# Optimization experiments

Hardware: AMD Instinct MI355X
Metric: run time of the kernel (lower is better)

Reference implementation:

```python
import jax, jax.numpy as jnp
import numpy as np

B, T, H_IMG, HID, ACT = 128, 100, 72, 512, 2


def _conv(x, w, b, stride, pad):
    y = jax.lax.conv_general_dilated(
        x, w, (stride, stride), [(pad, pad), (pad, pad)],
        dimension_numbers=('NCHW', 'OIHW', 'NCHW'))
    return y + b[None, :, None, None]


def _encode(images, cw1, cb1, cw2, cb2, cw3, cb3, fw1, fb1, fw2, fb2, fw3, fb3):
    relu = jax.nn.relu
    x = relu(_conv(images, cw1, cb1, 3, 2))   # [B,64,24,24]
    x = relu(_conv(x, cw2, cb2, 3, 2))        # [B,64,9,9]
    x = relu(_conv(x, cw3, cb3, 3, 2))        # [B,64,4,4]
    x = x.reshape(x.shape[0], -1)             # [B,1024]
    x = relu(x @ fw1.T + fb1)
    x = relu(x @ fw2.T + fb2)
    return x @ fw3.T + fb3                    # [B,512]


def _gru(actions, h0, w_ih, w_hh, b_ih, b_hh):
    # precompute input projections for all steps: [T,B,3H]
    gi = jnp.einsum('btd,gd->tbg', actions, w_ih) + b_ih

    def step(h, gi_t):
        gh = h @ w_hh.T + b_hh
        i_r, i_i, i_n = jnp.split(gi_t, 3, axis=-1)
        h_r, h_i, h_n = jnp.split(gh, 3, axis=-1)
        r = jax.nn.sigmoid(i_r + h_r)
        z = jax.nn.sigmoid(i_i + h_i)
        n = jnp.tanh(i_n + r * h_n)
        hy = n + z * (h - n)
        return hy, hy

    hT, outs = jax.lax.scan(step, h0, gi)
    return jnp.transpose(outs, (1, 0, 2)), hT  # batch_first output


def setup_inputs() -> dict:
    key = jax.random.key(0)
    ks = jax.random.split(key, 16)
    s = 0.05
    return {
        'images': jax.random.normal(ks[0], (B, 3, H_IMG, H_IMG), jnp.float32),
        'actions': jax.random.normal(ks[1], (B, T, ACT), jnp.float32),
        'cw1': jax.random.normal(ks[2], (64, 3, 5, 5), jnp.float32) * s,
        'cb1': jax.random.normal(ks[3], (64,), jnp.float32) * s,
        'cw2': jax.random.normal(ks[4], (64, 64, 3, 3), jnp.float32) * s,
        'cb2': jax.random.normal(ks[5], (64,), jnp.float32) * s,
        'cw3': jax.random.normal(ks[6], (64, 64, 3, 3), jnp.float32) * s,
        'cb3': jax.random.normal(ks[7], (64,), jnp.float32) * s,
        'fw1': jax.random.normal(ks[8], (1024, 1024), jnp.float32) * 0.02,
        'fb1': jax.random.normal(ks[9], (1024,), jnp.float32) * 0.02,
        'fw2': jax.random.normal(ks[10], (512, 1024), jnp.float32) * 0.02,
        'fb2': jax.random.normal(ks[11], (512,), jnp.float32) * 0.02,
        'fw3': jax.random.normal(ks[12], (512, 512), jnp.float32) * 0.02,
        'fb3': jax.random.normal(ks[13], (512,), jnp.float32) * 0.02,
        'w_ih': jax.random.normal(ks[14], (3 * HID, ACT), jnp.float32) * 0.05,
        'w_hh': jax.random.normal(ks[15], (3 * HID, HID), jnp.float32) * 0.04,
        'b_ih': jnp.zeros((3 * HID,), jnp.float32),
        'b_hh': jnp.zeros((3 * HID,), jnp.float32),
    }


def reference(images, actions, cw1, cb1, cw2, cb2, cw3, cb3,
              fw1, fb1, fw2, fb2, fw3, fb3, w_ih, w_hh, b_ih, b_hh):
    # Encode the start image to a 512-d representation (BigBasicConv),
    # then integrate the action sequence with the hand-rolled GRU,
    # initial hidden state = start representation.
    h0 = _encode(images, cw1, cb1, cw2, cb2, cw3, cb3,
                 fw1, fb1, fw2, fb2, fw3, fb3)
    output, hT = _gru(actions, h0, w_ih, w_hh, b_ih, b_hh)
    return output, hT
```

## Files before the change

kernel.cpp:

```cpp
#include <hip/hip_runtime.h>
#include <cstdint>

#define BB   128
#define TT   100
#define HID  512

typedef __attribute__((ext_vector_type(4))) float f32x4;
typedef __attribute__((ext_vector_type(2))) float f32x2;
typedef __attribute__((ext_vector_type(8))) short short8;
typedef __attribute__((ext_vector_type(4))) short short4_t;

__device__ __forceinline__ short f2bf(float x) {
  unsigned u = __float_as_uint(x);
  unsigned r = (u + 0x7fffu + ((u >> 16) & 1u)) >> 16;
  return (short)r;
}
__device__ __forceinline__ float bf2f(short s) {
  return __uint_as_float(((unsigned)(unsigned short)s) << 16);
}

__global__ __launch_bounds__(256) void wsplit_k(const float* __restrict__ w,
                                                unsigned short* __restrict__ hi,
                                                unsigned short* __restrict__ lo,
                                                int nq) {
  int i = blockIdx.x * 256 + threadIdx.x;
  const int stride = gridDim.x * 256;
  for (; i < nq; i += stride) {
    f32x4 v = *(const f32x4*)(w + 4 * (long)i);
    short4_t h, l;
    #pragma unroll
    for (int c = 0; c < 4; c++) {
      short hh = f2bf(v[c]); h[c] = hh; l[c] = f2bf(v[c] - bf2f(hh));
    }
    *(short4_t*)(hi + 4 * (long)i) = h;
    *(short4_t*)(lo + 4 * (long)i) = l;
  }
}


__global__ __launch_bounds__(192) void conv1_k(const float* __restrict__ in,
                                               const float* __restrict__ w,
                                               const float* __restrict__ bias,
                                               float* __restrict__ out) {
  const int b = blockIdx.x / 24, oy = blockIdx.x % 24;
  __shared__ __attribute__((aligned(16))) float in_s[3][5][76];
  __shared__ __attribute__((aligned(16))) float ws[64][76];
  const int tid = threadIdx.x;
  for (int i = tid; i < 3 * 5 * 76; i += 192) {
    int ic = i / 380, rem = i % 380, r = rem / 76, p = rem % 76;
    int iy = oy * 3 + r - 2, ix = p - 2;
    in_s[ic][r][p] = (iy >= 0 && iy < 72 && ix >= 0 && ix < 72)
                       ? in[((long)(b * 3 + ic) * 72 + iy) * 72 + ix] : 0.f;
  }
  for (int i = tid; i < 64 * 75; i += 192) ws[i / 75][i % 75] = w[i];
  __syncthreads();

  const int ox2 = tid % 12;
  const int og = tid / 12;
  float strip[15][8];
  #pragma unroll
  for (int ic = 0; ic < 3; ic++)
    #pragma unroll
    for (int ky = 0; ky < 5; ky++) {
      const float* bp = &in_s[ic][ky][6 * ox2];
      #pragma unroll
      for (int h = 0; h < 4; h++) {
        f32x2 u = *(const f32x2*)(bp + 2 * h);
        strip[ic * 5 + ky][2 * h] = u[0];
        strip[ic * 5 + ky][2 * h + 1] = u[1];
      }
    }

  #pragma unroll
  for (int j = 0; j < 4; j++) {
    const int oc = og + 16 * j;
    float s0 = bias[oc], s1 = bias[oc];
    const float* wrow = ws[oc];
    #pragma unroll
    for (int k4 = 0; k4 < 18; k4++) {
      f32x4 wq = *(const f32x4*)(wrow + 4 * k4);
      #pragma unroll
      for (int q = 0; q < 4; q++) {
        const int k = 4 * k4 + q, i5 = k / 5, kx = k % 5;
        s0 += strip[i5][kx] * wq[q];
        s1 += strip[i5][kx + 3] * wq[q];
      }
    }
    s0 += strip[14][2] * wrow[72]; s1 += strip[14][5] * wrow[72];
    s0 += strip[14][3] * wrow[73]; s1 += strip[14][6] * wrow[73];
    s0 += strip[14][4] * wrow[74]; s1 += strip[14][7] * wrow[74];
    long o = ((long)(b * 64 + oc) * 24 + oy) * 24 + 2 * ox2;
    out[o] = fmaxf(s0, 0.f);
    out[o + 1] = fmaxf(s1, 0.f);
  }
}

template <int IC, int IH, int IW, int OC, int OH, int OW>
__global__ void convs3(const float* __restrict__ in, const float* __restrict__ w,
                       const float* __restrict__ bias, float* __restrict__ out) {
  const int b = blockIdx.x / OH, oy = blockIdx.x % OH;
  constexpr int PW = 3 * OW;
  constexpr int NT = (OC / 2) * OW;
  __shared__ __attribute__((aligned(16))) float in_s[8][3][PW];
  __shared__ __attribute__((aligned(16))) float w_s[OC][100];
  const int tid = threadIdx.x;
  const int oc = tid / OW, ox = tid % OW;
  float s0 = bias[oc], s1 = bias[oc + OC / 2];
  for (int cc = 0; cc < IC; cc += 8) {
    __syncthreads();
    for (int i = tid; i < 8 * 3 * PW; i += NT) {
      int ic = i / (3 * PW), r = (i / PW) % 3, p = i % PW;
      int iy = oy * 3 - 2 + r, ix = p - 2;
      in_s[ic][r][p] = (iy >= 0 && iy < IH && ix >= 0 && ix < IW)
                         ? in[((long)(b * IC + cc + ic) * IH + iy) * IW + ix] : 0.f;
    }
    for (int i = tid; i < OC * 8 * 9; i += NT) {
      int o = i / 72, r = i % 72;
      w_s[o][(r / 9) * 12 + (r % 9)] = w[(long)(o * IC + cc + r / 9) * 9 + r % 9];
    }
    __syncthreads();
    #pragma unroll
    for (int ic = 0; ic < 8; ic++) {
      const float* wr0 = &w_s[oc][ic * 12];
      const float* wr1 = &w_s[oc + OC / 2][ic * 12];
      f32x4 wa = *(const f32x4*)wr0, wb = *(const f32x4*)(wr0 + 4);
      f32x4 va = *(const f32x4*)wr1, vb = *(const f32x4*)(wr1 + 4);
      float wA[9] = {wa[0], wa[1], wa[2], wa[3], wb[0], wb[1], wb[2], wb[3], wr0[8]};
      float wB[9] = {va[0], va[1], va[2], va[3], vb[0], vb[1], vb[2], vb[3], wr1[8]};
      #pragma unroll
      for (int ky = 0; ky < 3; ky++)
        #pragma unroll
        for (int kx = 0; kx < 3; kx++) {
          float iv = in_s[ic][ky][ox * 3 + kx];
          s0 += iv * wA[ky * 3 + kx];
          s1 += iv * wB[ky * 3 + kx];
        }
    }
  }
  out[((long)(b * OC + oc) * OH + oy) * OW + ox] = fmaxf(s0, 0.f);
  out[((long)(b * OC + oc + OC / 2) * OH + oy) * OW + ox] = fmaxf(s1, 0.f);
}

template <int K, int N, bool RELU>
__global__ __launch_bounds__(128) void fc_mfma(const float* __restrict__ A,
                                               const unsigned short* __restrict__ wh,
                                               const unsigned short* __restrict__ wl,
                                               const float* __restrict__ bias,
                                               float* __restrict__ C) {
  const int nb = N / 32;
  const int rb = (blockIdx.x / nb) * 16, cb = (blockIdx.x % nb) * 32;
  __shared__ __attribute__((aligned(16))) short A_hi[16][K + 8];
  __shared__ __attribute__((aligned(16))) short A_lo[16][K + 8];
  const int tid = threadIdx.x;
  const int wv = tid >> 6, lane = tid & 63, n16 = lane & 15, quad = lane >> 4;

  for (int i = tid; i < 16 * (K / 4); i += 128) {
    int row = i / (K / 4), q = i % (K / 4);
    f32x4 v = *(const f32x4*)(A + (long)(rb + row) * K + 4 * q);
    short4_t sh, sl;
    #pragma unroll
    for (int c = 0; c < 4; c++) {
      short hh = f2bf(v[c]); sh[c] = hh; sl[c] = f2bf(v[c] - bf2f(hh));
    }
    *(short4_t*)&A_hi[row][4 * q] = sh;
    *(short4_t*)&A_lo[row][4 * q] = sl;
  }
  __syncthreads();

  const int col = cb + wv * 16 + n16;
  f32x4 a0 = {0.f, 0.f, 0.f, 0.f}, a1 = a0, a2 = a0;
  constexpr int NP = K / 512;
  #pragma unroll 1
  for (int p = 0; p < NP; p++) {
    short8 fh[16], fl[16];
    const unsigned short* wb0 = wh + (long)col * K + p * 512 + quad * 8;
    const unsigned short* wb1 = wl + (long)col * K + p * 512 + quad * 8;
    #pragma unroll
    for (int ks = 0; ks < 16; ks++) {
      fh[ks] = *(const short8*)(wb0 + ks * 32);
      fl[ks] = *(const short8*)(wb1 + ks * 32);
    }
    #pragma unroll
    for (int ks = 0; ks < 16; ks++) {
      short8 ah = *(const short8*)&A_hi[n16][p * 512 + ks * 32 + quad * 8];
      short8 al = *(const short8*)&A_lo[n16][p * 512 + ks * 32 + quad * 8];
      a0 = __builtin_amdgcn_mfma_f32_16x16x32_bf16(ah, fh[ks], a0, 0, 0, 0);
      a1 = __builtin_amdgcn_mfma_f32_16x16x32_bf16(al, fh[ks], a1, 0, 0, 0);
      a2 = __builtin_amdgcn_mfma_f32_16x16x32_bf16(ah, fl[ks], a2, 0, 0, 0);
    }
  }
  const float bv = bias[col];
  #pragma unroll
  for (int r = 0; r < 4; r++) {
    float v = a0[r] + a1[r] + a2[r] + bv;
    if (RELU) v = fmaxf(v, 0.f);
    C[(long)(rb + quad * 4 + r) * N + col] = v;
  }
}

__global__ __launch_bounds__(192, 1) void gru_k(
    const float* __restrict__ actions, const float* __restrict__ w_ih,
    const float* __restrict__ w_hh, const float* __restrict__ b_ih,
    const float* __restrict__ b_hh, const float* __restrict__ h0,
    float* __restrict__ out, float* __restrict__ hT, unsigned* __restrict__ bar) {
  const int bg = blockIdx.x >> 5;
  const int hg = blockIdx.x & 31;
  const int tid = threadIdx.x;
  const int wv = tid >> 6;
  const int lane = tid & 63;
  const int n16 = lane & 15;
  const int quad = lane >> 4;

  __shared__ short h_hi[16][520];
  __shared__ short h_lo[16][520];
  __shared__ float act_s[16][2 * TT];
  __shared__ float gh_s[3][16][17];
  __shared__ float bih_s[48], bhh_s[48], wih0_s[48], wih1_s[48];

  short8 whi[16], wlo[16];
  {
    const int grow = wv * HID + hg * 16 + n16;
    const float* wr = w_hh + (long)grow * HID + quad * 8;
    #pragma unroll
    for (int ks = 0; ks < 16; ks++) {
      f32x4 v0 = *(const f32x4*)(wr + ks * 32);
      f32x4 v1 = *(const f32x4*)(wr + ks * 32 + 4);
      short8 hi, lo;
      #pragma unroll
      for (int j = 0; j < 4; j++) {
        short h1 = f2bf(v0[j]); hi[j] = h1;     lo[j] = f2bf(v0[j] - bf2f(h1));
        short h2 = f2bf(v1[j]); hi[j + 4] = h2; lo[j + 4] = f2bf(v1[j] - bf2f(h2));
      }
      whi[ks] = hi; wlo[ks] = lo;
    }
  }
  for (int i = tid; i < 48; i += 192) {
    int row = (i >> 4) * HID + hg * 16 + (i & 15);
    bih_s[i] = b_ih[row];
    bhh_s[i] = b_hh[row];
    wih0_s[i] = w_ih[row * 2];
    wih1_s[i] = w_ih[row * 2 + 1];
  }
  for (int i = tid; i < 16 * 2 * TT; i += 192) {
    int m = i / (2 * TT), r = i % (2 * TT);
    act_s[m][r] = actions[(long)(bg * 16 + m) * (2 * TT) + r];
  }
  for (int i = tid; i < 2048; i += 192) {
    int m = i >> 7, k4 = (i & 127) << 2;
    f32x4 v = *(const f32x4*)(h0 + (long)(bg * 16 + m) * HID + k4);
    short4_t sh, sl;
    #pragma unroll
    for (int c2 = 0; c2 < 4; c2++) {
      short hh = f2bf(v[c2]); sh[c2] = hh; sl[c2] = f2bf(v[c2] - bf2f(hh));
    }
    *(short4_t*)&h_hi[m][k4] = sh;
    *(short4_t*)&h_lo[m][k4] = sl;
  }
  __syncthreads();

  unsigned* my_bar = bar + bg * 32;

  #pragma unroll 1
  for (int t = 0; t < TT; t++) {
    f32x4 a0 = {0.f, 0.f, 0.f, 0.f}, a1 = a0, a2 = a0;
    #pragma unroll
    for (int ks = 0; ks < 16; ks++) {
      short8 ah = *(const short8*)&h_hi[n16][ks * 32 + quad * 8];
      short8 al = *(const short8*)&h_lo[n16][ks * 32 + quad * 8];
      a0 = __builtin_amdgcn_mfma_f32_16x16x32_bf16(ah, whi[ks], a0, 0, 0, 0);
      a1 = __builtin_amdgcn_mfma_f32_16x16x32_bf16(al, whi[ks], a1, 0, 0, 0);
      a2 = __builtin_amdgcn_mfma_f32_16x16x32_bf16(ah, wlo[ks], a2, 0, 0, 0);
    }
    #pragma unroll
    for (int r = 0; r < 4; r++)
      gh_s[wv][quad * 4 + r][n16] = a0[r] + a1[r] + a2[r];
    __syncthreads();

    if (tid < 128) {
      const int m = tid >> 3;
      const int n0 = (tid & 7) << 1;
      const float x0 = act_s[m][2 * t], x1 = act_s[m][2 * t + 1];
      float hy[2];
      #pragma unroll
      for (int q = 0; q < 2; q++) {
        int n = n0 + q;
        float hr = gh_s[0][m][n] + bhh_s[n];
        float hz = gh_s[1][m][n] + bhh_s[16 + n];
        float hn = gh_s[2][m][n] + bhh_s[32 + n];
        float ir = x0 * wih0_s[n]      + x1 * wih1_s[n]      + bih_s[n];
        float iz = x0 * wih0_s[16 + n] + x1 * wih1_s[16 + n] + bih_s[16 + n];
        float in_ = x0 * wih0_s[32 + n] + x1 * wih1_s[32 + n] + bih_s[32 + n];
        float rg = 1.f / (1.f + __expf(-(ir + hr)));
        float zg = 1.f / (1.f + __expf(-(iz + hz)));
        float nx = in_ + rg * hn;
        float ng = 1.f - 2.f / (__expf(2.f * nx) + 1.f);
        float hprev = bf2f(h_hi[m][hg * 16 + n]) + bf2f(h_lo[m][hg * 16 + n]);
        hy[q] = ng + zg * (hprev - ng);
      }
      unsigned long long pack = (unsigned long long)__float_as_uint(hy[0]) |
                                ((unsigned long long)__float_as_uint(hy[1]) << 32);
      __hip_atomic_store(
          (unsigned long long*)&out[((long)(bg * 16 + m) * TT + t) * HID + hg * 16 + n0],
          pack, __ATOMIC_RELAXED, __HIP_MEMORY_SCOPE_AGENT);
      if (t == TT - 1)
        *(unsigned long long*)&hT[(long)(bg * 16 + m) * HID + hg * 16 + n0] = pack;
    }
    __syncthreads();

    if (t < TT - 1) {
      if (tid == 0) {
        const unsigned target = 32u * (unsigned)(t + 1);
        unsigned prev = __hip_atomic_fetch_add(my_bar, 1u, __ATOMIC_RELAXED,
                                               __HIP_MEMORY_SCOPE_AGENT);
        if (prev + 1u < target) {
          while (__hip_atomic_load(my_bar, __ATOMIC_RELAXED,
                                   __HIP_MEMORY_SCOPE_AGENT) < target)
            __builtin_amdgcn_s_sleep(1);
        }
      }
      __syncthreads();
      unsigned long long vbuf[22];
      #pragma unroll
      for (int u = 0; u < 21; u++) {
        int i = tid + u * 192;
        int m = i >> 8, j = (i & 255) << 1;
        vbuf[u] = __hip_atomic_load(
            (const unsigned long long*)(out + ((long)(bg * 16 + m) * TT + t) * HID + j),
            __ATOMIC_RELAXED, __HIP_MEMORY_SCOPE_AGENT);
      }
      if (tid < 64) {
        int i = 4032 + tid;
        int m = i >> 8, j = (i & 255) << 1;
        vbuf[21] = __hip_atomic_load(
            (const unsigned long long*)(out + ((long)(bg * 16 + m) * TT + t) * HID + j),
            __ATOMIC_RELAXED, __HIP_MEMORY_SCOPE_AGENT);
      }
      #pragma unroll
      for (int u = 0; u < 21; u++) {
        int i = tid + u * 192;
        int m = i >> 8, j = (i & 255) << 1;
        unsigned long long v = vbuf[u];
        float f0 = __uint_as_float((unsigned)v);
        float f1 = __uint_as_float((unsigned)(v >> 32));
        short s0 = f2bf(f0);
        h_hi[m][j] = s0; h_lo[m][j] = f2bf(f0 - bf2f(s0));
        short s1 = f2bf(f1);
        h_hi[m][j + 1] = s1; h_lo[m][j + 1] = f2bf(f1 - bf2f(s1));
      }
      if (tid < 64) {
        int i = 4032 + tid;
        int m = i >> 8, j = (i & 255) << 1;
        unsigned long long v = vbuf[21];
        float f0 = __uint_as_float((unsigned)v);
        float f1 = __uint_as_float((unsigned)(v >> 32));
        short s0 = f2bf(f0);
        h_hi[m][j] = s0; h_lo[m][j] = f2bf(f0 - bf2f(s0));
        short s1 = f2bf(f1);
        h_hi[m][j + 1] = s1; h_lo[m][j + 1] = f2bf(f1 - bf2f(s1));
      }
      __syncthreads();
    }
  }
}

extern "C" void kernel_launch(void* const* d_in, const int* in_sizes, int n_in,
                              void* d_out, int out_size, void* d_ws, size_t ws_size,
                              hipStream_t stream) {
  const float* images  = (const float*)d_in[0];
  const float* actions = (const float*)d_in[1];
  const float* cw1 = (const float*)d_in[2];
  const float* cb1 = (const float*)d_in[3];
  const float* cw2 = (const float*)d_in[4];
  const float* cb2 = (const float*)d_in[5];
  const float* cw3 = (const float*)d_in[6];
  const float* cb3 = (const float*)d_in[7];
  const float* fw1 = (const float*)d_in[8];
  const float* fb1 = (const float*)d_in[9];
  const float* fw2 = (const float*)d_in[10];
  const float* fb2 = (const float*)d_in[11];
  const float* fw3 = (const float*)d_in[12];
  const float* fb3 = (const float*)d_in[13];
  const float* w_ih = (const float*)d_in[14];
  const float* w_hh = (const float*)d_in[15];
  const float* b_ih = (const float*)d_in[16];
  const float* b_hh = (const float*)d_in[17];

  char* ws = (char*)d_ws;
  unsigned* bar = (unsigned*)ws;
  float* a1 = (float*)(ws + 1024);
  float* a2 = a1 + (long)128 * 64 * 576;
  float* a3 = a2 + (long)128 * 64 * 81;
  float* f1 = a3 + (long)128 * 1024;
  float* f2 = f1 + (long)128 * 1024;
  float* h0 = f2 + (long)128 * 512;
  unsigned short* wfh1 = (unsigned short*)(h0 + 65536);
  unsigned short* wfl1 = wfh1 + (long)1048576;
  unsigned short* wfh2 = wfl1 + (long)1048576;
  unsigned short* wfl2 = wfh2 + (long)524288;
  unsigned short* wfh3 = wfl2 + (long)524288;
  unsigned short* wfl3 = wfh3 + (long)262144;

  float* out = (float*)d_out;
  float* hT  = out + (long)BB * TT * HID;

  hipMemsetAsync(bar, 0, 1024, stream);
  wsplit_k<<<256, 256, 0, stream>>>(fw1, wfh1, wfl1, 262144);
  wsplit_k<<<128, 256, 0, stream>>>(fw2, wfh2, wfl2, 131072);
  wsplit_k<<<64, 256, 0, stream>>>(fw3, wfh3, wfl3, 65536);
  conv1_k<<<128 * 24, 192, 0, stream>>>(images, cw1, cb1, a1);
  convs3<64, 24, 24, 64, 9, 9><<<128 * 9, 288, 0, stream>>>(a1, cw2, cb2, a2);
  convs3<64, 9, 9, 64, 4, 4><<<128 * 4, 128, 0, stream>>>(a2, cw3, cb3, a3);
  fc_mfma<1024, 1024, true><<<256, 128, 0, stream>>>(a3, wfh1, wfl1, fb1, f1);
  fc_mfma<1024, 512, true><<<128, 128, 0, stream>>>(f1, wfh2, wfl2, fb2, f2);
  fc_mfma<512, 512, false><<<128, 128, 0, stream>>>(f2, wfh3, wfl3, fb3, h0);
  gru_k<<<256, 192, 0, stream>>>(actions, w_ih, w_hh, b_ih, b_hh, h0, out, hT, bar);
}
```

Before: 645.1 us.

## Exchange GRU hidden state as pre-split bf16 planes read directly into MFMA fragments

Each GRU block now publishes its new hidden slice as double-buffered bf16 hi/lo planes in global memory. The next step loads the MFMA A-fragments straight from those planes, which removes the per-step fp32 reload of the full hidden state, the bf16 split and the LDS staging pass. Work across the three waves is also rearranged: wave 0 multiplies h_hi by W_hi, wave 1 h_lo by W_hi and wave 2 h_hi by W_lo, each covering all three gates, and the partial sums are added in shared memory. Previous hidden values stay in registers, and an extra wsplit launch splits h0 into hi/lo. The cost is more weight registers per wave and uncached agent-scope global loads sitting on the critical path of every step.

```diff
diff --git a/kernel.cpp b/kernel.cpp
--- a/kernel.cpp
+++ b/kernel.cpp
@@ -202,36 +202,41 @@
     const float* __restrict__ actions, const float* __restrict__ w_ih,
     const float* __restrict__ w_hh, const float* __restrict__ b_ih,
     const float* __restrict__ b_hh, const float* __restrict__ h0,
-    float* __restrict__ out, float* __restrict__ hT, unsigned* __restrict__ bar) {
+    float* __restrict__ out, float* __restrict__ hT, unsigned* __restrict__ bar,
+    unsigned short* __restrict__ xh, unsigned short* __restrict__ xl) {
   const int bg = blockIdx.x >> 5;
   const int hg = blockIdx.x & 31;
   const int tid = threadIdx.x;
-  const int wv = tid >> 6;
+  const int ch = tid >> 6;
   const int lane = tid & 63;
   const int n16 = lane & 15;
   const int quad = lane >> 4;
-
-  __shared__ short h_hi[16][520];
-  __shared__ short h_lo[16][520];
+  const long PLANE = (long)BB * HID;
+
   __shared__ float act_s[16][2 * TT];
-  __shared__ float gh_s[3][16][17];
+  __shared__ float gh_s[3][16][52];
   __shared__ float bih_s[48], bhh_s[48], wih0_s[48], wih1_s[48];
 
-  short8 whi[16], wlo[16];
+  short8 wfrag[3][16];
   {
-    const int grow = wv * HID + hg * 16 + n16;
-    const float* wr = w_hh + (long)grow * HID + quad * 8;
-    #pragma unroll
-    for (int ks = 0; ks < 16; ks++) {
-      f32x4 v0 = *(const f32x4*)(wr + ks * 32);
-      f32x4 v1 = *(const f32x4*)(wr + ks * 32 + 4);
-      short8 hi, lo;
+    #pragma unroll
+    for (int g = 0; g < 3; g++) {
+      const int grow = g * HID + hg * 16 + n16;
+      const float* wr = w_hh + (long)grow * HID + quad * 8;
       #pragma unroll
-      for (int j = 0; j < 4; j++) {
-        short h1 = f2bf(v0[j]); hi[j] = h1;     lo[j] = f2bf(v0[j] - bf2f(h1));
-        short h2 = f2bf(v1[j]); hi[j + 4] = h2; lo[j + 4] = f2bf(v1[j] - bf2f(h2));
-      }
-      whi[ks] = hi; wlo[ks] = lo;
+      for (int ks = 0; ks < 16; ks++) {
+        f32x4 v0 = *(const f32x4*)(wr + ks * 32);
+        f32x4 v1 = *(const f32x4*)(wr + ks * 32 + 4);
+        short8 f;
+        #pragma unroll
+        for (int j = 0; j < 4; j++) {
+          float x0 = v0[j], x1 = v1[j];
+          short hh0 = f2bf(x0), hh1 = f2bf(x1);
+          f[j]     = (ch == 2) ? f2bf(x0 - bf2f(hh0)) : hh0;
+          f[j + 4] = (ch == 2) ? f2bf(x1 - bf2f(hh1)) : hh1;
+        }
+        wfrag[g][ks] = f;
+      }
     }
   }
   for (int i = tid; i < 48; i += 192) {
@@ -245,35 +250,45 @@
     int m = i / (2 * TT), r = i % (2 * TT);
     act_s[m][r] = actions[(long)(bg * 16 + m) * (2 * TT) + r];
   }
-  for (int i = tid; i < 2048; i += 192) {
-    int m = i >> 7, k4 = (i & 127) << 2;
-    f32x4 v = *(const f32x4*)(h0 + (long)(bg * 16 + m) * HID + k4);
-    short4_t sh, sl;
-    #pragma unroll
-    for (int c2 = 0; c2 < 4; c2++) {
-      short hh = f2bf(v[c2]); sh[c2] = hh; sl[c2] = f2bf(v[c2] - bf2f(hh));
-    }
-    *(short4_t*)&h_hi[m][k4] = sh;
-    *(short4_t*)&h_lo[m][k4] = sl;
+  float hp0 = 0.f, hp1 = 0.f;
+  if (tid < 128) {
+    const int m = tid >> 3, n0 = (tid & 7) << 1;
+    f32x2 u = *(const f32x2*)(h0 + (long)(bg * 16 + m) * HID + hg * 16 + n0);
+    hp0 = u[0]; hp1 = u[1];
   }
   __syncthreads();
 
   unsigned* my_bar = bar + bg * 32;
+  const unsigned short* xa = (ch == 1) ? xl : xh;
+  const long lane_off = ((long)(bg * 16 + n16) << 9) + quad * 8;
 
   #pragma unroll 1
   for (int t = 0; t < TT; t++) {
+    const unsigned long long* fp =
+        (const unsigned long long*)(xa + (t & 1) * PLANE + lane_off);
+    unsigned long long fb[16][2];
+    #pragma unroll
+    for (int ks = 0; ks < 16; ks++) {
+      fb[ks][0] = __hip_atomic_load(fp + ks * 8, __ATOMIC_RELAXED,
+                                    __HIP_MEMORY_SCOPE_AGENT);
+      fb[ks][1] = __hip_atomic_load(fp + ks * 8 + 1, __ATOMIC_RELAXED,
+                                    __HIP_MEMORY_SCOPE_AGENT);
+    }
     f32x4 a0 = {0.f, 0.f, 0.f, 0.f}, a1 = a0, a2 = a0;
     #pragma unroll
     for (int ks = 0; ks < 16; ks++) {
-      short8 ah = *(const short8*)&h_hi[n16][ks * 32 + quad * 8];
-      short8 al = *(const short8*)&h_lo[n16][ks * 32 + quad * 8];
-      a0 = __builtin_amdgcn_mfma_f32_16x16x32_bf16(ah, whi[ks], a0, 0, 0, 0);
-      a1 = __builtin_amdgcn_mfma_f32_16x16x32_bf16(al, whi[ks], a1, 0, 0, 0);
-      a2 = __builtin_amdgcn_mfma_f32_16x16x32_bf16(ah, wlo[ks], a2, 0, 0, 0);
-    }
-    #pragma unroll
-    for (int r = 0; r < 4; r++)
-      gh_s[wv][quad * 4 + r][n16] = a0[r] + a1[r] + a2[r];
+      union { unsigned long long q[2]; short8 s; } u;
+      u.q[0] = fb[ks][0]; u.q[1] = fb[ks][1];
+      a0 = __builtin_amdgcn_mfma_f32_16x16x32_bf16(u.s, wfrag[0][ks], a0, 0, 0, 0);
+      a1 = __builtin_amdgcn_mfma_f32_16x16x32_bf16(u.s, wfrag[1][ks], a1, 0, 0, 0);
+      a2 = __builtin_amdgcn_mfma_f32_16x16x32_bf16(u.s, wfrag[2][ks], a2, 0, 0, 0);
+    }
+    #pragma unroll
+    for (int r = 0; r < 4; r++) {
+      gh_s[ch][quad * 4 + r][n16]      = a0[r];
+      gh_s[ch][quad * 4 + r][16 + n16] = a1[r];
+      gh_s[ch][quad * 4 + r][32 + n16] = a2[r];
+    }
     __syncthreads();
 
     if (tid < 128) {
@@ -284,9 +299,9 @@
       #pragma unroll
       for (int q = 0; q < 2; q++) {
         int n = n0 + q;
-        float hr = gh_s[0][m][n] + bhh_s[n];
-        float hz = gh_s[1][m][n] + bhh_s[16 + n];
-        float hn = gh_s[2][m][n] + bhh_s[32 + n];
+        float hr = gh_s[0][m][n]      + gh_s[1][m][n]      + gh_s[2][m][n]      + bhh_s[n];
+        float hz = gh_s[0][m][16 + n] + gh_s[1][m][16 + n] + gh_s[2][m][16 + n] + bhh_s[16 + n];
+        float hn = gh_s[0][m][32 + n] + gh_s[1][m][32 + n] + gh_s[2][m][32 + n] + bhh_s[32 + n];
         float ir = x0 * wih0_s[n]      + x1 * wih1_s[n]      + bih_s[n];
         float iz = x0 * wih0_s[16 + n] + x1 * wih1_s[16 + n] + bih_s[16 + n];
         float in_ = x0 * wih0_s[32 + n] + x1 * wih1_s[32 + n] + bih_s[32 + n];
@@ -294,16 +309,29 @@
         float zg = 1.f / (1.f + __expf(-(iz + hz)));
         float nx = in_ + rg * hn;
         float ng = 1.f - 2.f / (__expf(2.f * nx) + 1.f);
-        float hprev = bf2f(h_hi[m][hg * 16 + n]) + bf2f(h_lo[m][hg * 16 + n]);
+        float hprev = q ? hp1 : hp0;
         hy[q] = ng + zg * (hprev - ng);
       }
+      hp0 = hy[0]; hp1 = hy[1];
       unsigned long long pack = (unsigned long long)__float_as_uint(hy[0]) |
                                 ((unsigned long long)__float_as_uint(hy[1]) << 32);
-      __hip_atomic_store(
-          (unsigned long long*)&out[((long)(bg * 16 + m) * TT + t) * HID + hg * 16 + n0],
-          pack, __ATOMIC_RELAXED, __HIP_MEMORY_SCOPE_AGENT);
-      if (t == TT - 1)
+      *(unsigned long long*)&out[((long)(bg * 16 + m) * TT + t) * HID + hg * 16 + n0] = pack;
+      if (t == TT - 1) {
         *(unsigned long long*)&hT[(long)(bg * 16 + m) * HID + hg * 16 + n0] = pack;
+      } else {
+        short s0h = f2bf(hy[0]), s1h = f2bf(hy[1]);
+        short s0l = f2bf(hy[0] - bf2f(s0h)), s1l = f2bf(hy[1] - bf2f(s1h));
+        unsigned hpk = (unsigned)(unsigned short)s0h |
+                       ((unsigned)(unsigned short)s1h << 16);
+        unsigned lpk = (unsigned)(unsigned short)s0l |
+                       ((unsigned)(unsigned short)s1l << 16);
+        const long xo = ((t + 1) & 1) * PLANE +
+                        ((long)(bg * 16 + m) << 9) + hg * 16 + n0;
+        __hip_atomic_store((unsigned*)(xh + xo), hpk, __ATOMIC_RELAXED,
+                           __HIP_MEMORY_SCOPE_AGENT);
+        __hip_atomic_store((unsigned*)(xl + xo), lpk, __ATOMIC_RELAXED,
+                           __HIP_MEMORY_SCOPE_AGENT);
+      }
     }
     __syncthreads();
 
@@ -317,46 +345,6 @@
                                    __HIP_MEMORY_SCOPE_AGENT) < target)
             __builtin_amdgcn_s_sleep(1);
         }
-      }
-      __syncthreads();
-      unsigned long long vbuf[22];
-      #pragma unroll
-      for (int u = 0; u < 21; u++) {
-        int i = tid + u * 192;
-        int m = i >> 8, j = (i & 255) << 1;
-        vbuf[u] = __hip_atomic_load(
-            (const unsigned long long*)(out + ((long)(bg * 16 + m) * TT + t) * HID + j),
-            __ATOMIC_RELAXED, __HIP_MEMORY_SCOPE_AGENT);
-      }
-      if (tid < 64) {
-        int i = 4032 + tid;
-        int m = i >> 8, j = (i & 255) << 1;
-        vbuf[21] = __hip_atomic_load(
-            (const unsigned long long*)(out + ((long)(bg * 16 + m) * TT + t) * HID + j),
-            __ATOMIC_RELAXED, __HIP_MEMORY_SCOPE_AGENT);
-      }
-      #pragma unroll
-      for (int u = 0; u < 21; u++) {
-        int i = tid + u * 192;
-        int m = i >> 8, j = (i & 255) << 1;
-        unsigned long long v = vbuf[u];
-        float f0 = __uint_as_float((unsigned)v);
-        float f1 = __uint_as_float((unsigned)(v >> 32));
-        short s0 = f2bf(f0);
-        h_hi[m][j] = s0; h_lo[m][j] = f2bf(f0 - bf2f(s0));
-        short s1 = f2bf(f1);
-        h_hi[m][j + 1] = s1; h_lo[m][j + 1] = f2bf(f1 - bf2f(s1));
-      }
-      if (tid < 64) {
-        int i = 4032 + tid;
-        int m = i >> 8, j = (i & 255) << 1;
-        unsigned long long v = vbuf[21];
-        float f0 = __uint_as_float((unsigned)v);
-        float f1 = __uint_as_float((unsigned)(v >> 32));
-        short s0 = f2bf(f0);
-        h_hi[m][j] = s0; h_lo[m][j] = f2bf(f0 - bf2f(s0));
-        short s1 = f2bf(f1);
-        h_hi[m][j + 1] = s1; h_lo[m][j + 1] = f2bf(f1 - bf2f(s1));
       }
       __syncthreads();
     }
@@ -399,6 +387,8 @@
   unsigned short* wfl2 = wfh2 + (long)524288;
   unsigned short* wfh3 = wfl2 + (long)524288;
   unsigned short* wfl3 = wfh3 + (long)262144;
+  unsigned short* xh = wfl3 + (long)262144;
+  unsigned short* xl = xh + (long)2 * 128 * 512;
 
   float* out = (float*)d_out;
   float* hT  = out + (long)BB * TT * HID;
@@ -413,5 +403,7 @@
   fc_mfma<1024, 1024, true><<<256, 128, 0, stream>>>(a3, wfh1, wfl1, fb1, f1);
   fc_mfma<1024, 512, true><<<128, 128, 0, stream>>>(f1, wfh2, wfl2, fb2, f2);
   fc_mfma<512, 512, false><<<128, 128, 0, stream>>>(f2, wfh3, wfl3, fb3, h0);
-  gru_k<<<256, 192, 0, stream>>>(actions, w_ih, w_hh, b_ih, b_hh, h0, out, hT, bar);
-}
+  wsplit_k<<<64, 256, 0, stream>>>(h0, xh, xl, 16384);
+  gru_k<<<256, 192, 0, stream>>>(actions, w_ih, w_hh, b_ih, b_hh, h0, out, hT,
+                                 bar, xh, xl);
+}
```

Result: slower. 783.2 us (+21.4%).

## Replace GRU atomic counter barrier with tagged double-buffered hidden-state exchange

Applied to the files above, without the earlier changes.

Drops the per-batch-group atomic counter barrier and the extra __syncthreads between GRU steps. Each block now publishes its new hidden-state slice to a double-buffered exchange buffer, pre-split into bf16 hi/lo pairs with a parity tag bit in the low mantissa bit. Consumers poll the tagged words directly until every tag matches, then unpack them into shared memory without redoing the split. The previous hidden value is also kept in registers instead of being rebuilt from shared memory. The cost is one low bit of the lo part per element and a second global write stream alongside the out writes.

```diff
diff --git a/kernel.cpp b/kernel.cpp
--- a/kernel.cpp
+++ b/kernel.cpp
@@ -9,6 +9,7 @@
 typedef __attribute__((ext_vector_type(2))) float f32x2;
 typedef __attribute__((ext_vector_type(8))) short short8;
 typedef __attribute__((ext_vector_type(4))) short short4_t;
+typedef unsigned long long ull;
 
 __device__ __forceinline__ short f2bf(float x) {
   unsigned u = __float_as_uint(x);
@@ -202,7 +203,8 @@
     const float* __restrict__ actions, const float* __restrict__ w_ih,
     const float* __restrict__ w_hh, const float* __restrict__ b_ih,
     const float* __restrict__ b_hh, const float* __restrict__ h0,
-    float* __restrict__ out, float* __restrict__ hT, unsigned* __restrict__ bar) {
+    float* __restrict__ out, float* __restrict__ hT,
+    unsigned* __restrict__ xb) {
   const int bg = blockIdx.x >> 5;
   const int hg = blockIdx.x & 31;
   const int tid = threadIdx.x;
@@ -256,9 +258,13 @@
     *(short4_t*)&h_hi[m][k4] = sh;
     *(short4_t*)&h_lo[m][k4] = sl;
   }
+  float hp0 = 0.f, hp1 = 0.f;
+  if (tid < 128) {
+    const int m = tid >> 3, n0 = (tid & 7) << 1;
+    f32x2 u = *(const f32x2*)(h0 + (long)(bg * 16 + m) * HID + hg * 16 + n0);
+    hp0 = u[0]; hp1 = u[1];
+  }
   __syncthreads();
-
-  unsigned* my_bar = bar + bg * 32;
 
   #pragma unroll 1
   for (int t = 0; t < TT; t++) {
@@ -275,6 +281,10 @@
     for (int r = 0; r < 4; r++)
       gh_s[wv][quad * 4 + r][n16] = a0[r] + a1[r] + a2[r];
     __syncthreads();
+
+    const int nt = t + 1;
+    const unsigned tagbit = (unsigned)((nt >> 1) & 1);
+    unsigned* xcur = xb + (nt & 1) * 65536;
 
     if (tid < 128) {
       const int m = tid >> 3;
@@ -294,69 +304,75 @@
         float zg = 1.f / (1.f + __expf(-(iz + hz)));
         float nx = in_ + rg * hn;
         float ng = 1.f - 2.f / (__expf(2.f * nx) + 1.f);
-        float hprev = bf2f(h_hi[m][hg * 16 + n]) + bf2f(h_lo[m][hg * 16 + n]);
+        float hprev = q ? hp1 : hp0;
         hy[q] = ng + zg * (hprev - ng);
       }
-      unsigned long long pack = (unsigned long long)__float_as_uint(hy[0]) |
-                                ((unsigned long long)__float_as_uint(hy[1]) << 32);
-      __hip_atomic_store(
-          (unsigned long long*)&out[((long)(bg * 16 + m) * TT + t) * HID + hg * 16 + n0],
-          pack, __ATOMIC_RELAXED, __HIP_MEMORY_SCOPE_AGENT);
-      if (t == TT - 1)
-        *(unsigned long long*)&hT[(long)(bg * 16 + m) * HID + hg * 16 + n0] = pack;
-    }
-    __syncthreads();
+      hp0 = hy[0]; hp1 = hy[1];
+      ull pack = (ull)__float_as_uint(hy[0]) |
+                 ((ull)__float_as_uint(hy[1]) << 32);
+      *(ull*)&out[((long)(bg * 16 + m) * TT + t) * HID + hg * 16 + n0] = pack;
+      if (t == TT - 1) {
+        *(ull*)&hT[(long)(bg * 16 + m) * HID + hg * 16 + n0] = pack;
+      } else {
+        short s0h = f2bf(hy[0]), s1h = f2bf(hy[1]);
+        short s0l = f2bf(hy[0] - bf2f(s0h)), s1l = f2bf(hy[1] - bf2f(s1h));
+        unsigned w0 = ((unsigned)(unsigned short)s0h << 16) |
+                      (((unsigned)(unsigned short)s0l) & 0xFFFEu) | tagbit;
+        unsigned w1 = ((unsigned)(unsigned short)s1h << 16) |
+                      (((unsigned)(unsigned short)s1l) & 0xFFFEu) | tagbit;
+        ull pk = (ull)w0 | ((ull)w1 << 32);
+        __hip_atomic_store(
+            (ull*)xcur + ((long)bg * 4096 + m * 256 + hg * 8 + (n0 >> 1)),
+            pk, __ATOMIC_RELAXED, __HIP_MEMORY_SCOPE_AGENT);
+      }
+    }
 
     if (t < TT - 1) {
-      if (tid == 0) {
-        const unsigned target = 32u * (unsigned)(t + 1);
-        unsigned prev = __hip_atomic_fetch_add(my_bar, 1u, __ATOMIC_RELAXED,
-                                               __HIP_MEMORY_SCOPE_AGENT);
-        if (prev + 1u < target) {
-          while (__hip_atomic_load(my_bar, __ATOMIC_RELAXED,
-                                   __HIP_MEMORY_SCOPE_AGENT) < target)
-            __builtin_amdgcn_s_sleep(1);
+      const ull* xq = (const ull*)xcur + (long)bg * 4096;
+      ull vb[22];
+      #pragma unroll
+      for (int u = 0; u < 21; u++)
+        vb[u] = __hip_atomic_load(xq + tid + u * 192, __ATOMIC_RELAXED,
+                                  __HIP_MEMORY_SCOPE_AGENT);
+      if (tid < 64)
+        vb[21] = __hip_atomic_load(xq + 4032 + tid, __ATOMIC_RELAXED,
+                                   __HIP_MEMORY_SCOPE_AGENT);
+      for (;;) {
+        unsigned bad = 0;
+        #pragma unroll
+        for (int u = 0; u < 21; u++) {
+          unsigned lo32 = (unsigned)vb[u], hi32 = (unsigned)(vb[u] >> 32);
+          if ((((lo32 ^ tagbit) | (hi32 ^ tagbit)) & 1u) != 0u) {
+            vb[u] = __hip_atomic_load(xq + tid + u * 192, __ATOMIC_RELAXED,
+                                      __HIP_MEMORY_SCOPE_AGENT);
+            bad = 1u;
+          }
         }
-      }
-      __syncthreads();
-      unsigned long long vbuf[22];
+        if (tid < 64) {
+          unsigned lo32 = (unsigned)vb[21], hi32 = (unsigned)(vb[21] >> 32);
+          if ((((lo32 ^ tagbit) | (hi32 ^ tagbit)) & 1u) != 0u) {
+            vb[21] = __hip_atomic_load(xq + 4032 + tid, __ATOMIC_RELAXED,
+                                       __HIP_MEMORY_SCOPE_AGENT);
+            bad = 1u;
+          }
+        }
+        if (!bad) break;
+        __builtin_amdgcn_s_sleep(1);
+      }
       #pragma unroll
       for (int u = 0; u < 21; u++) {
-        int i = tid + u * 192;
-        int m = i >> 8, j = (i & 255) << 1;
-        vbuf[u] = __hip_atomic_load(
-            (const unsigned long long*)(out + ((long)(bg * 16 + m) * TT + t) * HID + j),
-            __ATOMIC_RELAXED, __HIP_MEMORY_SCOPE_AGENT);
+        int c = tid + u * 192;
+        int m = c >> 8, j = (c & 255) << 1;
+        unsigned lo32 = (unsigned)vb[u], hi32 = (unsigned)(vb[u] >> 32);
+        *(unsigned*)&h_hi[m][j] = (lo32 >> 16) | (hi32 & 0xFFFF0000u);
+        *(unsigned*)&h_lo[m][j] = (lo32 & 0xFFFEu) | ((hi32 & 0xFFFEu) << 16);
       }
       if (tid < 64) {
-        int i = 4032 + tid;
-        int m = i >> 8, j = (i & 255) << 1;
-        vbuf[21] = __hip_atomic_load(
-            (const unsigned long long*)(out + ((long)(bg * 16 + m) * TT + t) * HID + j),
-            __ATOMIC_RELAXED, __HIP_MEMORY_SCOPE_AGENT);
-      }
-      #pragma unroll
-      for (int u = 0; u < 21; u++) {
-        int i = tid + u * 192;
-        int m = i >> 8, j = (i & 255) << 1;
-        unsigned long long v = vbuf[u];
-        float f0 = __uint_as_float((unsigned)v);
-        float f1 = __uint_as_float((unsigned)(v >> 32));
-        short s0 = f2bf(f0);
-        h_hi[m][j] = s0; h_lo[m][j] = f2bf(f0 - bf2f(s0));
-        short s1 = f2bf(f1);
-        h_hi[m][j + 1] = s1; h_lo[m][j + 1] = f2bf(f1 - bf2f(s1));
-      }
-      if (tid < 64) {
-        int i = 4032 + tid;
-        int m = i >> 8, j = (i & 255) << 1;
-        unsigned long long v = vbuf[21];
-        float f0 = __uint_as_float((unsigned)v);
-        float f1 = __uint_as_float((unsigned)(v >> 32));
-        short s0 = f2bf(f0);
-        h_hi[m][j] = s0; h_lo[m][j] = f2bf(f0 - bf2f(s0));
-        short s1 = f2bf(f1);
-        h_hi[m][j + 1] = s1; h_lo[m][j + 1] = f2bf(f1 - bf2f(s1));
+        int c = 4032 + tid;
+        int m = c >> 8, j = (c & 255) << 1;
+        unsigned lo32 = (unsigned)vb[21], hi32 = (unsigned)(vb[21] >> 32);
+        *(unsigned*)&h_hi[m][j] = (lo32 >> 16) | (hi32 & 0xFFFF0000u);
+        *(unsigned*)&h_lo[m][j] = (lo32 & 0xFFFEu) | ((hi32 & 0xFFFEu) << 16);
       }
       __syncthreads();
     }
@@ -386,7 +402,6 @@
   const float* b_hh = (const float*)d_in[17];
 
   char* ws = (char*)d_ws;
-  unsigned* bar = (unsigned*)ws;
   float* a1 = (float*)(ws + 1024);
   float* a2 = a1 + (long)128 * 64 * 576;
   float* a3 = a2 + (long)128 * 64 * 81;
@@ -399,11 +414,13 @@
   unsigned short* wfl2 = wfh2 + (long)524288;
   unsigned short* wfh3 = wfl2 + (long)524288;
   unsigned short* wfl3 = wfh3 + (long)262144;
+  unsigned* xb = (unsigned*)(wfl3 + 262144);
 
   float* out = (float*)d_out;
   float* hT  = out + (long)BB * TT * HID;
 
-  hipMemsetAsync(bar, 0, 1024, stream);
+  hipMemsetAsync(xb, 0x00, 65536 * 4, stream);
+  hipMemsetAsync(xb + 65536, 0x01, 65536 * 4, stream);
   wsplit_k<<<256, 256, 0, stream>>>(fw1, wfh1, wfl1, 262144);
   wsplit_k<<<128, 256, 0, stream>>>(fw2, wfh2, wfl2, 131072);
   wsplit_k<<<64, 256, 0, stream>>>(fw3, wfh3, wfl3, 65536);
@@ -413,5 +430,6 @@
   fc_mfma<1024, 1024, true><<<256, 128, 0, stream>>>(a3, wfh1, wfl1, fb1, f1);
   fc_mfma<1024, 512, true><<<128, 128, 0, stream>>>(f1, wfh2, wfl2, fb2, f2);
   fc_mfma<512, 512, false><<<128, 128, 0, stream>>>(f2, wfh3, wfl3, fb3, h0);
-  gru_k<<<256, 192, 0, stream>>>(actions, w_ih, w_hh, b_ih, b_hh, h0, out, hT, bar);
-}
+  gru_k<<<256, 192, 0, stream>>>(actions, w_ih, w_hh, b_ih, b_hh, h0, out, hT,
+                                 xb);
+}
```

Result: slower. 826.3 us (+28.1%).
